# Kernel tuning notes

Hardware: AMD Instinct MI355X
Metric: run time of the kernel (lower is better)

## Reference

```python
import jax, jax.numpy as jnp
from jax import lax
import numpy as np

B, T, D, H, OUT = 128, 1024, 256, 256, 2


def _rnn_layer(inp, W_xh, W_hh, b):
    # inp: [B, T, Din]; returns [B, T, H]
    h0 = jnp.zeros((inp.shape[0], W_hh.shape[0]), inp.dtype)

    def step(h, x_t):
        h_new = jnp.tanh(x_t @ W_xh.T + h @ W_hh.T + b)
        return h_new, h_new

    _, ys = lax.scan(step, h0, jnp.swapaxes(inp, 0, 1))  # ys: [T, B, H]
    return jnp.swapaxes(ys, 0, 1)


def setup_inputs() -> dict:
    key = jax.random.key(0)
    ks = jax.random.split(key, 8)
    s_in = 1.0 / np.sqrt(H)  # torch nn.RNN init scale
    x = jax.random.normal(ks[0], (B, T, D), dtype=jnp.float32)
    W_xh0 = jax.random.uniform(ks[1], (H, D), jnp.float32, -s_in, s_in)
    W_hh0 = jax.random.uniform(ks[2], (H, H), jnp.float32, -s_in, s_in)
    b0 = jax.random.uniform(ks[3], (H,), jnp.float32, -s_in, s_in)
    W_xh1 = jax.random.uniform(ks[4], (H, H), jnp.float32, -s_in, s_in)
    W_hh1 = jax.random.uniform(ks[5], (H, H), jnp.float32, -s_in, s_in)
    b1 = jax.random.uniform(ks[6], (H,), jnp.float32, -s_in, s_in)
    fc_w = jax.random.uniform(ks[7], (OUT, H), jnp.float32, -s_in, s_in)
    fc_b = jnp.zeros((OUT,), jnp.float32)
    return {"x": x, "W_xh0": W_xh0, "W_hh0": W_hh0, "b0": b0,
            "W_xh1": W_xh1, "W_hh1": W_hh1, "b1": b1,
            "fc_w": fc_w, "fc_b": fc_b}


def reference(x, W_xh0, W_hh0, b0, W_xh1, W_hh1, b1, fc_w, fc_b):
    h1 = _rnn_layer(x, W_xh0, W_hh0, b0)   # [B, T, H]
    h2 = _rnn_layer(h1, W_xh1, W_hh1, b1)  # [B, T, H]
    # linear head on last timestep
    return h2[:, -1, :] @ fc_w.T + fc_b    # [B, OUT]
```

## Files before the change

### kernel.cpp

```cpp
#include <hip/hip_runtime.h>

#define Bsz 128
#define Tn  1024
#define Dn  256
#define Hn  256

typedef _Float16 f16;
typedef _Float16 f16x4 __attribute__((ext_vector_type(4)));
typedef _Float16 f16x8 __attribute__((ext_vector_type(8)));
typedef float f32x4 __attribute__((ext_vector_type(4)));

#define MF(A, B, C) __builtin_amdgcn_mfma_f32_16x16x32_f16((A), (B), (C), 0, 0, 0)

__device__ __forceinline__ float tanh_fast(float x) {
    float e = __builtin_amdgcn_exp2f(x * 2.88539008177793f);
    return 1.0f - 2.0f * __builtin_amdgcn_rcpf(e + 1.0f);
}

__device__ __forceinline__ void wg_barrier() {
    asm volatile("s_waitcnt lgkmcnt(0)\n\ts_barrier" ::: "memory");
}


__global__ __launch_bounds__(512, 1) void k_xproj(
    const float* __restrict__ x, const float* __restrict__ W,
    const float* __restrict__ bias, float* __restrict__ preT)
{
    const int tid  = threadIdx.x;
    const int lane = tid & 63, l15 = lane & 15, quad = lane >> 4;
    const int w    = tid >> 6;
    const int colbase = w * 32;

    f16x8 wf[2][8];
    #pragma unroll
    for (int jn = 0; jn < 2; jn++) {
        int j = colbase + jn * 16 + l15;
        #pragma unroll
        for (int kk = 0; kk < 8; kk++) {
            const float* wp = W + (size_t)j * Dn + kk * 32 + quad * 8;
            float4 a = *(const float4*)(wp);
            float4 b = *(const float4*)(wp + 4);
            wf[jn][kk] = (f16x8){ (f16)a.x, (f16)a.y, (f16)a.z, (f16)a.w,
                                  (f16)b.x, (f16)b.y, (f16)b.z, (f16)b.w };
        }
    }
    float4 bx[2];
    #pragma unroll
    for (int jn = 0; jn < 2; jn++)
        bx[jn] = *(const float4*)(bias + colbase + jn * 16 + quad * 4);

    #pragma unroll 1
    for (int tt = 0; tt < 4; tt++) {
        const int t = blockIdx.x * 4 + tt;
        #pragma unroll
        for (int bblk = 0; bblk < 8; bblk++) {
            const float* xp = x + ((size_t)(bblk * 16 + l15) * Tn + t) * Dn + quad * 8;
            f16x8 xb[8];
            #pragma unroll
            for (int kk = 0; kk < 8; kk++) {
                float4 a = *(const float4*)(xp + kk * 32);
                float4 b = *(const float4*)(xp + kk * 32 + 4);
                xb[kk] = (f16x8){ (f16)a.x, (f16)a.y, (f16)a.z, (f16)a.w,
                                  (f16)b.x, (f16)b.y, (f16)b.z, (f16)b.w };
            }
            f32x4 acc0 = (f32x4){bx[0].x, bx[0].y, bx[0].z, bx[0].w};
            f32x4 acc1 = (f32x4){bx[1].x, bx[1].y, bx[1].z, bx[1].w};
            #pragma unroll
            for (int kk = 0; kk < 8; kk++) {
                acc0 = MF(wf[0][kk], xb[kk], acc0);
                acc1 = MF(wf[1][kk], xb[kk], acc1);
            }
            float* pp = preT + ((size_t)t * Bsz + bblk * 16 + l15) * Hn
                             + colbase + quad * 4;
            *(f32x4*)(pp)      = acc0;
            *(f32x4*)(pp + 16) = acc1;
        }
    }
}

__global__ __launch_bounds__(512, 1) void k_fused(
    const float* __restrict__ Whh0, const float* __restrict__ Wxh1,
    const float* __restrict__ Whh1, const float* __restrict__ b1v,
    const float* __restrict__ fcw,  const float* __restrict__ fcb,
    const float* __restrict__ preT, float* __restrict__ out)
{
    __shared__ __align__(16) f16 h1f[2][4096];
    __shared__ __align__(16) f16 h2f[2][4096];

    const int tid  = threadIdx.x;
    const int lane = tid & 63, l15 = lane & 15, quad = lane >> 4;
    const int w    = tid >> 6;
    const int colbase = w * 32;
    const int bg   = blockIdx.x * 16;

    for (int i = tid; i < 4096; i += 512) {
        h1f[0][i] = (f16)0.0f; h1f[1][i] = (f16)0.0f;
        h2f[0][i] = (f16)0.0f; h2f[1][i] = (f16)0.0f;
    }

    f16x8 wh0[2][8], wx[2][8], wh1[2][8];
    #pragma unroll
    for (int jn = 0; jn < 2; jn++) {
        int j = colbase + jn * 16 + l15;
        #pragma unroll
        for (int kk = 0; kk < 8; kk++)
            #pragma unroll
            for (int e = 0; e < 8; e++) {
                int o = (int)((size_t)j * Hn + kk * 32 + quad * 8 + e);
                wh0[jn][kk][e] = (f16)Whh0[o];
                wx [jn][kk][e] = (f16)Wxh1[o];
                wh1[jn][kk][e] = (f16)Whh1[o];
            }
    }
    float4 bi[2];
    #pragma unroll
    for (int jn = 0; jn < 2; jn++)
        bi[jn] = *(const float4*)(b1v + colbase + jn * 16 + quad * 4);

    int wroff[2];
    #pragma unroll
    for (int jn = 0; jn < 2; jn++) {
        int n0 = colbase + jn * 16 + quad * 4;
        wroff[jn] = (n0 >> 5) * 512 + ((n0 >> 3) & 3) * 128 + l15 * 8 + (n0 & 7);
    }

    const float* pp = preT + ((size_t)(bg + l15)) * Hn + colbase + quad * 4;

    f32x4 pnv[2];
    pnv[0] = *(const f32x4*)(pp);
    pnv[1] = *(const f32x4*)(pp + 16);
    __syncthreads();

#define FSTEP_FULL(PR, I, TF) { \
    f32x4 accA[2]; \
    accA[0] = pnv[0]; accA[1] = pnv[1]; \
    pnv[0] = *(const f32x4*)(pp + (size_t)(TF) * (Bsz * Hn)); \
    pnv[1] = *(const f32x4*)(pp + (size_t)(TF) * (Bsz * Hn) + 16); \
    f16x8 hb1[8]; \
    _Pragma("unroll") for (int kk = 0; kk < 8; kk++) { \
        hb1[kk] = *(const f16x8*)(&h1f[(PR)^1][kk * 512 + lane * 8]); \
        accA[0] = MF(wh0[0][kk], hb1[kk], accA[0]); \
        accA[1] = MF(wh0[1][kk], hb1[kk], accA[1]); \
    } \
     \
    _Pragma("unroll") for (int jn = 0; jn < 2; jn++) { \
        f16x4 t1v = { (f16)tanh_fast(accA[jn][0]), (f16)tanh_fast(accA[jn][1]), \
                      (f16)tanh_fast(accA[jn][2]), (f16)tanh_fast(accA[jn][3]) }; \
        *(f16x4*)(&h1f[(PR)][wroff[jn]]) = t1v; \
    } \
    f32x4 accB[2]; \
    _Pragma("unroll") for (int jn = 0; jn < 2; jn++) \
        accB[jn] = (f32x4){bi[jn].x, bi[jn].y, bi[jn].z, bi[jn].w}; \
    _Pragma("unroll") for (int kk = 0; kk < 8; kk++) { \
        f16x8 hb2 = *(const f16x8*)(&h2f[(PR)][kk * 512 + lane * 8]); \
        accB[0] = MF(wx [0][kk], hb1[kk], accB[0]); \
        accB[1] = MF(wx [1][kk], hb1[kk], accB[1]); \
        accB[0] = MF(wh1[0][kk], hb2, accB[0]); \
        accB[1] = MF(wh1[1][kk], hb2, accB[1]); \
    } \
    _Pragma("unroll") for (int jn = 0; jn < 2; jn++) { \
        f16x4 t2v = { (f16)tanh_fast(accB[jn][0]), (f16)tanh_fast(accB[jn][1]), \
                      (f16)tanh_fast(accB[jn][2]), (f16)tanh_fast(accB[jn][3]) }; \
        *(f16x4*)(&h2f[(PR)^1][wroff[jn]]) = t2v; \
    } \
    wg_barrier(); \
}

    {
        f32x4 accA[2];
        accA[0] = pnv[0]; accA[1] = pnv[1];
        pnv[0] = *(const f32x4*)(pp + (size_t)1 * (Bsz * Hn));
        pnv[1] = *(const f32x4*)(pp + (size_t)1 * (Bsz * Hn) + 16);
        #pragma unroll
        for (int kk = 0; kk < 8; kk++) {
            f16x8 hb1 = *(const f16x8*)(&h1f[1][kk * 512 + lane * 8]);
            accA[0] = MF(wh0[0][kk], hb1, accA[0]);
            accA[1] = MF(wh0[1][kk], hb1, accA[1]);
        }
        #pragma unroll
        for (int jn = 0; jn < 2; jn++) {
            f16x4 t1v = { (f16)tanh_fast(accA[jn][0]), (f16)tanh_fast(accA[jn][1]),
                          (f16)tanh_fast(accA[jn][2]), (f16)tanh_fast(accA[jn][3]) };
            *(f16x4*)(&h1f[0][wroff[jn]]) = t1v;
        }
        wg_barrier();
    }

    #pragma unroll 1
    for (int tp = 0; tp < 511; ++tp) {
        const int t1 = 2 * tp + 1;
        FSTEP_FULL(1, t1, (t1 + 1))
        FSTEP_FULL(0, (t1 + 1), (t1 + 2))
    }
    FSTEP_FULL(1, 1023, 1023)
#undef FSTEP_FULL

    {
        f32x4 accB[2];
        #pragma unroll
        for (int jn = 0; jn < 2; jn++)
            accB[jn] = (f32x4){bi[jn].x, bi[jn].y, bi[jn].z, bi[jn].w};
        #pragma unroll
        for (int kk = 0; kk < 8; kk++) {
            f16x8 hb1 = *(const f16x8*)(&h1f[1][kk * 512 + lane * 8]);
            f16x8 hb2 = *(const f16x8*)(&h2f[0][kk * 512 + lane * 8]);
            accB[0] = MF(wx [0][kk], hb1, accB[0]);
            accB[1] = MF(wx [1][kk], hb1, accB[1]);
            accB[0] = MF(wh1[0][kk], hb2, accB[0]);
            accB[1] = MF(wh1[1][kk], hb2, accB[1]);
        }
        #pragma unroll
        for (int jn = 0; jn < 2; jn++) {
            f16x4 t2v = { (f16)tanh_fast(accB[jn][0]), (f16)tanh_fast(accB[jn][1]),
                          (f16)tanh_fast(accB[jn][2]), (f16)tanh_fast(accB[jn][3]) };
            *(f16x4*)(&h2f[1][wroff[jn]]) = t2v;
        }
        wg_barrier();
    }

    if (tid < 256) {
        const int bl = tid >> 4, o = (tid >> 3) & 1, kc = tid & 7;
        float s = 0.f;
        #pragma unroll
        for (int kq = 0; kq < 32; kq++) {
            int k = kc * 32 + kq;
            f16 hv = h2f[1][(k >> 5) * 512 + ((k >> 3) & 3) * 128 + bl * 8 + (k & 7)];
            s += (float)hv * fcw[o * Hn + k];
        }
        s += __shfl_down(s, 4);
        s += __shfl_down(s, 2);
        s += __shfl_down(s, 1);
        if (kc == 0)
            out[(bg + bl) * 2 + o] = s + fcb[o];
    }
}

extern "C" void kernel_launch(void* const* d_in, const int* in_sizes, int n_in,
                              void* d_out, int out_size, void* d_ws, size_t ws_size,
                              hipStream_t stream) {
    const float* x    = (const float*)d_in[0];
    const float* Wxh0 = (const float*)d_in[1];
    const float* Whh0 = (const float*)d_in[2];
    const float* b0   = (const float*)d_in[3];
    const float* Wxh1 = (const float*)d_in[4];
    const float* Whh1 = (const float*)d_in[5];
    const float* b1   = (const float*)d_in[6];
    const float* fcw  = (const float*)d_in[7];
    const float* fcb  = (const float*)d_in[8];
    float* out = (float*)d_out;

    float* preT = (float*)d_ws;

    k_xproj<<<dim3(256), dim3(512), 0, stream>>>(x, Wxh0, b0, preT);
    k_fused<<<dim3(Bsz / 16), dim3(512), 0, stream>>>(Whh0, Wxh1, Whh1, b1,
                                                      fcw, fcb, preT, out);
}
```

Before: 1.455 ms.

## Pre-convert x to fp16 and restructure input projection with LDS-staged tiles

Adds a separate kernel that converts x to fp16 in a global buffer. The input-projection kernel is reorganised into 1024 blocks of 256 threads, each covering 16 batch rows by 8 timesteps. Each block stages its fp16 x tile into shared memory with coalesced loads, and each wave keeps 64 output columns of weights in registers. The goal is to stop the old kernel's strided fp32 reads of x, which were converted per wave, and to raise occupancy. The cost is an extra full pass over x, plus a 64 MB fp16 scratch buffer and a third launch.

Result: faster. 1.375 ms (-5.5%).

```diff
diff --git a/kernel.cpp b/kernel.cpp
--- a/kernel.cpp
+++ b/kernel.cpp
@@ -12,6 +12,8 @@
 
 #define MF(A, B, C) __builtin_amdgcn_mfma_f32_16x16x32_f16((A), (B), (C), 0, 0, 0)
 
+__device__ __align__(16) f16 g_x16[(size_t)Bsz * Tn * Dn];
+
 __device__ __forceinline__ float tanh_fast(float x) {
     float e = __builtin_amdgcn_exp2f(x * 2.88539008177793f);
     return 1.0f - 2.0f * __builtin_amdgcn_rcpf(e + 1.0f);
@@ -21,20 +23,37 @@
     asm volatile("s_waitcnt lgkmcnt(0)\n\ts_barrier" ::: "memory");
 }
 
-
-__global__ __launch_bounds__(512, 1) void k_xproj(
-    const float* __restrict__ x, const float* __restrict__ W,
-    const float* __restrict__ bias, float* __restrict__ preT)
+__global__ __launch_bounds__(256, 4) void k_cvt(const float* __restrict__ x)
 {
+    const size_t total = (size_t)Bsz * Tn * Dn;
+    size_t i = ((size_t)blockIdx.x * 256 + threadIdx.x) * 8;
+    const size_t stride = (size_t)gridDim.x * 256 * 8;
+    for (; i < total; i += stride) {
+        float4 a = *(const float4*)(x + i);
+        float4 b = *(const float4*)(x + i + 4);
+        f16x8 v = { (f16)a.x, (f16)a.y, (f16)a.z, (f16)a.w,
+                    (f16)b.x, (f16)b.y, (f16)b.z, (f16)b.w };
+        *(f16x8*)(g_x16 + i) = v;
+    }
+}
+
+__global__ __launch_bounds__(256, 2) void k_xproj(
+    const float* __restrict__ W, const float* __restrict__ bias,
+    float* __restrict__ preT)
+{
+    __shared__ __align__(16) f16 xs[8 * 4096];
+
     const int tid  = threadIdx.x;
     const int lane = tid & 63, l15 = lane & 15, quad = lane >> 4;
     const int w    = tid >> 6;
-    const int colbase = w * 32;
-
-    f16x8 wf[2][8];
-    #pragma unroll
-    for (int jn = 0; jn < 2; jn++) {
-        int j = colbase + jn * 16 + l15;
+    const int bgi  = blockIdx.x >> 7;
+    const int tc   = blockIdx.x & 127;
+    const int t0 = tc * 8, brange = bgi * 16;
+
+    f16x8 wf[4][8];
+    #pragma unroll
+    for (int jn = 0; jn < 4; jn++) {
+        int j = w * 64 + jn * 16 + l15;
         #pragma unroll
         for (int kk = 0; kk < 8; kk++) {
             const float* wp = W + (size_t)j * Dn + kk * 32 + quad * 8;
@@ -44,36 +63,42 @@
                                   (f16)b.x, (f16)b.y, (f16)b.z, (f16)b.w };
         }
     }
-    float4 bx[2];
-    #pragma unroll
-    for (int jn = 0; jn < 2; jn++)
-        bx[jn] = *(const float4*)(bias + colbase + jn * 16 + quad * 4);
+    float4 bx[4];
+    #pragma unroll
+    for (int jn = 0; jn < 4; jn++)
+        bx[jn] = *(const float4*)(bias + w * 64 + jn * 16 + quad * 4);
+
+    f16x8 stg[16];
+    #pragma unroll
+    for (int c = 0; c < 16; c++) {
+        int L = (c * 256 + tid) * 8;
+        int t = L >> 12, kk = (L >> 9) & 7, qs = (L >> 7) & 3, bs = (L >> 3) & 15;
+        stg[c] = *(const f16x8*)(g_x16 +
+                    ((size_t)(brange + bs) * Tn + (t0 + t)) * Dn + kk * 32 + qs * 8);
+    }
+    #pragma unroll
+    for (int c = 0; c < 16; c++)
+        *(f16x8*)(&xs[(c * 256 + tid) * 8]) = stg[c];
+    __syncthreads();
 
     #pragma unroll 1
-    for (int tt = 0; tt < 4; tt++) {
-        const int t = blockIdx.x * 4 + tt;
-        #pragma unroll
-        for (int bblk = 0; bblk < 8; bblk++) {
-            const float* xp = x + ((size_t)(bblk * 16 + l15) * Tn + t) * Dn + quad * 8;
-            f16x8 xb[8];
+    for (int t = 0; t < 8; t++) {
+        f32x4 acc[4];
+        #pragma unroll
+        for (int jn = 0; jn < 4; jn++)
+            acc[jn] = (f32x4){bx[jn].x, bx[jn].y, bx[jn].z, bx[jn].w};
+        #pragma unroll
+        for (int kk = 0; kk < 8; kk++) {
+            f16x8 xb = *(const f16x8*)(&xs[t * 4096 + kk * 512 + lane * 8]);
             #pragma unroll
-            for (int kk = 0; kk < 8; kk++) {
-                float4 a = *(const float4*)(xp + kk * 32);
-                float4 b = *(const float4*)(xp + kk * 32 + 4);
-                xb[kk] = (f16x8){ (f16)a.x, (f16)a.y, (f16)a.z, (f16)a.w,
-                                  (f16)b.x, (f16)b.y, (f16)b.z, (f16)b.w };
-            }
-            f32x4 acc0 = (f32x4){bx[0].x, bx[0].y, bx[0].z, bx[0].w};
-            f32x4 acc1 = (f32x4){bx[1].x, bx[1].y, bx[1].z, bx[1].w};
-            #pragma unroll
-            for (int kk = 0; kk < 8; kk++) {
-                acc0 = MF(wf[0][kk], xb[kk], acc0);
-                acc1 = MF(wf[1][kk], xb[kk], acc1);
-            }
-            float* pp = preT + ((size_t)t * Bsz + bblk * 16 + l15) * Hn
-                             + colbase + quad * 4;
-            *(f32x4*)(pp)      = acc0;
-            *(f32x4*)(pp + 16) = acc1;
+            for (int jn = 0; jn < 4; jn++)
+                acc[jn] = MF(wf[jn][kk], xb, acc[jn]);
+        }
+        #pragma unroll
+        for (int jn = 0; jn < 4; jn++) {
+            int j0 = w * 64 + jn * 16 + quad * 4;
+            *(f32x4*)(preT + ((size_t)(t0 + t) * Bsz + brange + l15) * Hn + j0)
+                = acc[jn];
         }
     }
 }
@@ -251,7 +276,8 @@
 
     float* preT = (float*)d_ws;
 
-    k_xproj<<<dim3(256), dim3(512), 0, stream>>>(x, Wxh0, b0, preT);
+    k_cvt  <<<dim3(2048), dim3(256), 0, stream>>>(x);
+    k_xproj<<<dim3(1024), dim3(256), 0, stream>>>(Wxh0, b0, preT);
     k_fused<<<dim3(Bsz / 16), dim3(512), 0, stream>>>(Whh0, Wxh1, Whh1, b1,
                                                       fcw, fcb, preT, out);
 }
```
